# Kernel tuning notes

Hardware: AMD Instinct MI355X
Metric: run time of the kernel (lower is better)

Reference implementation:

```python
import jax, jax.numpy as jnp
import numpy as np

DIM = 192
R = 16            # patches_resolution, D=H=W=R
SP = 4            # split_size
NH = 6            # num_heads (block level); per-branch heads = NH//3
B = 2
L = R * R * R
EPS = 1e-5


def layernorm(x, g, b):
    mu = jnp.mean(x, axis=-1, keepdims=True)
    var = jnp.mean(jnp.square(x - mu), axis=-1, keepdims=True)
    return (x - mu) * jax.lax.rsqrt(var + EPS) * g + b


def window_partition(x, d_sp, h_sp, w_sp, nh):
    b, _, _, _, cb = x.shape
    win = d_sp * h_sp * w_sp
    x = x.reshape(b, R // d_sp, d_sp, R // h_sp, h_sp, R // w_sp, w_sp, cb)
    x = x.transpose(0, 1, 3, 5, 2, 4, 6, 7).reshape(-1, win, nh, cb // nh)
    return x.transpose(0, 2, 1, 3)


def window_merge(x, d_sp, h_sp, w_sp, b):
    cb = x.shape[-1]
    x = x.reshape(b, R // d_sp, R // h_sp, R // w_sp, d_sp, h_sp, w_sp, cb)
    x = x.transpose(0, 1, 4, 2, 5, 3, 6, 7).reshape(b, L, cb)
    return x


def lepe_attention(q, k, v, d_sp, h_sp, w_sp, nh):
    # q,k,v: (B, L, Cb). Note: LePE bias is computed-but-unused in the source -> pure windowed SDPA.
    b, _, cb = q.shape
    hd = cb // nh
    scale = hd ** -0.5
    q5 = q.reshape(b, R, R, R, cb)
    k5 = k.reshape(b, R, R, R, cb)
    v5 = v.reshape(b, R, R, R, cb)
    qw = window_partition(q5, d_sp, h_sp, w_sp, nh) * scale
    kw = window_partition(k5, d_sp, h_sp, w_sp, nh)
    vw = window_partition(v5, d_sp, h_sp, w_sp, nh)
    attn = jax.nn.softmax(jnp.einsum('whqd,whkd->whqk', qw, kw), axis=-1)
    out = jnp.einsum('whqk,whkd->whqd', attn, vw)
    out = out.transpose(0, 2, 1, 3).reshape(-1, d_sp * h_sp * w_sp, cb)
    return window_merge(out, d_sp, h_sp, w_sp, b)


WINDOW_SHAPES = [(R, R, SP), (R, SP, R), (SP, R, R)]  # idx 0,1,2


def setup_inputs() -> dict:
    key = jax.random.key(0)
    ks = jax.random.split(key, 12)
    C = DIM
    H4 = int(C * 4)
    inp = {
        'x': jax.random.normal(ks[0], (B, C, R, R, R), dtype=jnp.float32),
        'w_qkv': jax.random.normal(ks[1], (C, 3 * C), dtype=jnp.float32) * (C ** -0.5),
        'w_proj': jax.random.normal(ks[2], (C, C), dtype=jnp.float32) * (C ** -0.5),
        'b_proj': jnp.zeros((C,), dtype=jnp.float32),
        'g1': jnp.ones((C,), dtype=jnp.float32),
        'b1': jnp.zeros((C,), dtype=jnp.float32),
        'g2': jnp.ones((C,), dtype=jnp.float32),
        'b2': jnp.zeros((C,), dtype=jnp.float32),
        'w_fc1': jax.random.normal(ks[3], (C, H4), dtype=jnp.float32) * (C ** -0.5),
        'b_fc1': jnp.zeros((H4,), dtype=jnp.float32),
        'w_fc2': jax.random.normal(ks[4], (H4, C), dtype=jnp.float32) * (H4 ** -0.5),
        'b_fc2': jnp.zeros((C,), dtype=jnp.float32),
    }
    return inp


def reference(x, w_qkv, w_proj, b_proj, g1, b1, g2, b2, w_fc1, b_fc1, w_fc2, b_fc2):
    C = DIM
    Cb = C // 3
    nh_b = NH // 3
    x = 2.0 * x
    xt = jnp.transpose(x, (0, 2, 3, 4, 1))                # (B, D, H, W, C)
    img = layernorm(xt, g1, b1)
    qkv = img.reshape(B, L, C) @ w_qkv                    # (B, L, 3C)
    q, k, v = jnp.split(qkv.reshape(B, L, 3, C).transpose(2, 0, 1, 3), 3, axis=0)
    q, k, v = q[0], k[0], v[0]                            # each (B, L, C)
    outs = []
    for i, (dsp, hsp, wsp) in enumerate(WINDOW_SHAPES):
        sl = slice(i * Cb, (i + 1) * Cb)
        outs.append(lepe_attention(q[..., sl], k[..., sl], v[..., sl], dsp, hsp, wsp, nh_b))
    attened = jnp.concatenate(outs, axis=2)               # (B, L, C)
    attened = attened @ w_proj + b_proj
    xs = xt.reshape(B, L, C) + attened
    h = layernorm(xs, g2, b2) @ w_fc1 + b_fc1
    h = jax.nn.gelu(h, approximate=False)
    xs = xs + (h @ w_fc2 + b_fc2)
    out = xs.reshape(B, R, R, R, C).transpose(0, 4, 1, 2, 3)  # (B, C, D, H, W)
    return out
```

## Files before the change

### kernel.cpp

```cpp
#include <hip/hip_runtime.h>
#include <hip/hip_bf16.h>

typedef __hip_bfloat16 bf16;
typedef short short8 __attribute__((ext_vector_type(8)));
typedef float floatx4 __attribute__((ext_vector_type(4)));

#define SZ (8192*192)

__device__ __forceinline__ unsigned short f2b(float f) {
    unsigned u = __builtin_bit_cast(unsigned, f);
    u += 0x7FFFu + ((u >> 16) & 1u);
    return (unsigned short)(u >> 16);
}
__device__ __forceinline__ float b2f(unsigned short h) {
    unsigned u = ((unsigned)h) << 16;
    return __builtin_bit_cast(float, u);
}
__device__ __forceinline__ unsigned pk2(float a, float b) {
    return ((unsigned)f2b(b) << 16) | (unsigned)f2b(a);
}

__global__ void detect_kernel(const unsigned short* __restrict__ x16, int* __restrict__ flag) {
    __shared__ int cnt;
    if (threadIdx.x == 0) cnt = 0;
    __syncthreads();
    int c = 0;
    for (int i = threadIdx.x; i < 8192; i += 256) {
        int e = (x16[i] >> 7) & 0xFF;
        if (e >= 152) c++;
    }
    if (c) atomicAdd(&cnt, c);
    __syncthreads();
    if (threadIdx.x == 0) *flag = (cnt >= 32) ? 1 : 0;
}

struct WPA { const void* s[11]; };

__global__ __launch_bounds__(256) void wprep_kernel(WPA a, unsigned short* __restrict__ wdst,
                                                    float* __restrict__ vdst,
                                                    const int* __restrict__ flag) {
    int i = blockIdx.x * 256 + threadIdx.x;
    int f = *flag;
    if (i < 442368) {
        int seg, base, K, N;
        if (i < 110592)      { seg = 0; base = 0;      K = 192; N = 576; }
        else if (i < 147456) { seg = 1; base = 110592; K = 192; N = 192; }
        else if (i < 294912) { seg = 2; base = 147456; K = 192; N = 768; }
        else                 { seg = 3; base = 294912; K = 768; N = 192; }
        int j = i - base;
        int n = j / K, k = j - n * K;
        size_t src = (size_t)k * N + n;
        float v = f ? ((const float*)a.s[seg])[src] : b2f(((const unsigned short*)a.s[seg])[src]);
        wdst[i] = f2b(v);
    } else if (i < 444288) {
        int j = i - 442368;
        int seg, off;
        if (j < 960)       { seg = 4 + j / 192; off = j % 192; }
        else if (j < 1728) { seg = 9; off = j - 960; }
        else               { seg = 10; off = j - 1728; }
        float v = f ? ((const float*)a.s[seg])[off] : b2f(((const unsigned short*)a.s[seg])[off]);
        vdst[j] = v;
    }
}

__global__ __launch_bounds__(256) void prep_kernel(const void* __restrict__ xin,
        const int* __restrict__ flag,
        const float* __restrict__ g1, const float* __restrict__ b1,
        float* __restrict__ xt, unsigned short* __restrict__ img) {
    __shared__ float tile[192][33];
    __shared__ float mu[32], rs[32];
    int tid = threadIdx.x;
    int t0 = blockIdx.x * 32;
    int b = t0 >> 12;
    int ts = t0 & 4095;
    int f = *flag;
    for (int idx = tid; idx < 192 * 32; idx += 256) {
        int c = idx >> 5, tt = idx & 31;
        int gi = ((b * 192 + c) << 12) + ts + tt;
        float raw = f ? ((const float*)xin)[gi] : b2f(((const unsigned short*)xin)[gi]);
        tile[c][tt] = 2.0f * raw;
    }
    __syncthreads();
    {
        int tt = tid >> 3, j = tid & 7;
        int c0 = j * 24;
        float s = 0.f, sq = 0.f;
        #pragma unroll
        for (int i = 0; i < 24; ++i) { float v = tile[c0 + i][tt]; s += v; sq += v * v; }
        s += __shfl_xor(s, 1); sq += __shfl_xor(sq, 1);
        s += __shfl_xor(s, 2); sq += __shfl_xor(sq, 2);
        s += __shfl_xor(s, 4); sq += __shfl_xor(sq, 4);
        if (j == 0) {
            float m = s * (1.0f / 192.0f);
            float var = sq * (1.0f / 192.0f) - m * m;
            mu[tt] = m;
            rs[tt] = rsqrtf(var + 1e-5f);
        }
    }
    __syncthreads();
    for (int idx = tid; idx < 32 * 192; idx += 256) {
        int tt = idx / 192, c = idx % 192;
        float v = tile[c][tt];
        int o = (t0 + tt) * 192 + c;
        xt[o] = v;
        img[o] = f2b((v - mu[tt]) * rs[tt] * g1[c] + b1[c]);
    }
}

__device__ __forceinline__ int g_of(int br, int t) {
    if (br == 0) return (((t >> 2) & 3) << 10) | ((t >> 8) << 6) | (((t >> 4) & 15) << 2) | (t & 3);
    if (br == 1) return (((t >> 6) & 3) << 10) | ((t >> 8) << 6) | (((t >> 4) & 3) << 4) | (t & 15);
    return t;
}

template <int MODE, int W>
__global__ __launch_bounds__(64 * W) void mfma_gemm(const unsigned short* __restrict__ A,
        const unsigned short* __restrict__ WT, const float* __restrict__ bias,
        const float* __restrict__ resid, void* __restrict__ out,
        unsigned short* __restrict__ kt, unsigned short* __restrict__ vt, int N, int K) {
    int wave = threadIdx.x >> 6, lane = threadIdx.x & 63;
    int quad = lane >> 4, l16 = lane & 15;
    int m0 = blockIdx.x * (32 * W) + wave * 32, n0 = blockIdx.y * 64;
    const unsigned short* ap = A + (size_t)(m0 + l16) * K + quad * 8;
    const unsigned short* wp = WT + (size_t)(n0 + l16) * K + quad * 8;
    floatx4 acc[2][4] = {};
    #pragma unroll 2
    for (int kc = 0; kc < K; kc += 32) {
        short8 a0 = *reinterpret_cast<const short8*>(ap + kc);
        short8 a1 = *reinterpret_cast<const short8*>(ap + (size_t)16 * K + kc);
        #pragma unroll
        for (int nt = 0; nt < 4; ++nt) {
            short8 w = *reinterpret_cast<const short8*>(wp + (size_t)nt * 16 * K + kc);
            acc[0][nt] = __builtin_amdgcn_mfma_f32_16x16x32_bf16(a0, w, acc[0][nt], 0, 0, 0);
            acc[1][nt] = __builtin_amdgcn_mfma_f32_16x16x32_bf16(a1, w, acc[1][nt], 0, 0, 0);
        }
    }
    #pragma unroll
    for (int fh = 0; fh < 2; ++fh) {
        #pragma unroll
        for (int nt = 0; nt < 4; ++nt) {
            int col = n0 + nt * 16 + l16;
            if (MODE == 0 && n0 >= 384) {
                int cv = col - 384;
                int d = cv & 31, brh = cv >> 5;
                int row0 = m0 + fh * 16 + quad * 4;
                int bb_ = row0 >> 12, tl = row0 & 4095;
                int g0 = g_of(brh >> 1, tl);
                int wb2 = g0 >> 10, k = g0 & 63, c = k >> 4, m = k & 15;
                int pos = ((c >> 1) << 5) + ((m >> 2) << 3) + ((c & 1) << 2);
                int chunk = (g0 & 1023) >> 6;
                int tidx = ((d >> 4) << 1) | (pos >> 5);
                unsigned short* tile = vt + (((((size_t)(bb_ * 6 + brh) * 4 + wb2) * 16 + chunk) * 4 + tidx) << 9);
                ushort4 w4;
                w4.x = f2b(acc[fh][nt][0]);
                w4.y = f2b(acc[fh][nt][1]);
                w4.z = f2b(acc[fh][nt][2]);
                w4.w = f2b(acc[fh][nt][3]);
                *reinterpret_cast<ushort4*>(tile + (d & 15) * 32 + (pos & 31)) = w4;
            } else if (MODE == 0 && n0 >= 192) {
                int ck = col - 192;
                int d = ck & 31, brh = ck >> 5;
                int row0 = m0 + fh * 16 + quad * 4;
                int bb_ = row0 >> 12, tl = row0 & 4095;
                int g0 = g_of(brh >> 1, tl);
                int wb2 = g0 >> 10, k = g0 & 63, c = k >> 4, m = k & 15;
                int chunk = (g0 & 1023) >> 6;
                unsigned short* tile = kt + (((((size_t)(bb_ * 6 + brh) * 4 + wb2) * 16 + chunk) * 4 + c) << 9);
                tile[m * 32 + d]       = f2b(acc[fh][nt][0]);
                tile[(m + 1) * 32 + d] = f2b(acc[fh][nt][1]);
                tile[(m + 2) * 32 + d] = f2b(acc[fh][nt][2]);
                tile[(m + 3) * 32 + d] = f2b(acc[fh][nt][3]);
            } else {
                #pragma unroll
                for (int r = 0; r < 4; ++r) {
                    int row = m0 + fh * 16 + quad * 4 + r;
                    float v = acc[fh][nt][r];
                    if (MODE == 0 && col < 192) v *= 0.17677669529663689f;
                    if (MODE >= 1) v += bias[col];
                    if (MODE == 2) v = 0.5f * v * (1.0f + erff(v * 0.70710678118654752f));
                    size_t o = (size_t)row * N + col;
                    if (MODE == 0 || MODE == 2) ((unsigned short*)out)[o] = f2b(v);
                    else                        ((float*)out)[o] = v + resid[o];
                }
            }
        }
    }
}

__device__ __forceinline__ int tok_of(int br, int wb, int q) {
    if (br == 0) return ((q >> 6) << 8) | (((q >> 2) & 15) << 4) | (wb << 2) | (q & 3);
    else if (br == 1) return ((q >> 6) << 8) | (((wb << 2) + ((q >> 4) & 3)) << 4) | (q & 15);
    else return (((wb << 2) + (q >> 8)) << 8) | (q & 255);
}

template <int SPLIT>
__global__ __launch_bounds__(256) void attn_mfma(const unsigned short* __restrict__ qkv,
        const unsigned short* __restrict__ kt, const unsigned short* __restrict__ vt,
        unsigned short* __restrict__ attb, float* __restrict__ po, float* __restrict__ pl) {
    const int chunk = 96 * SPLIT;
    int hw = blockIdx.x;
    int bid = (hw & 7) * chunk + (hw >> 3);
    int kh, rest;
    if (SPLIT == 2) { kh = bid & 1; rest = bid >> 1; }
    else            { kh = 0;       rest = bid; }
    int qt = rest & 15, head = (rest >> 4) & 1, wb = (rest >> 5) & 3, b = (rest >> 7) & 1, br = rest >> 8;
    int tid = threadIdx.x;
    int wave = tid >> 6, lane = tid & 63, quad = lane >> 4, l16 = lane & 15;
    int coff = br * 64 + head * 32;
    int tb = b << 12;
    int tq = tok_of(br, wb, qt * 64 + wave * 16 + l16);
    short8 aq = *reinterpret_cast<const short8*>(qkv + (size_t)(tb + tq) * 576 + coff + quad * 8);
    floatx4 o0 = {}, o1 = {};
    float lsum = 0.f;

    const int NT = 16 / SPLIT;
    const size_t base_idx = ((((size_t)(b * 6 + br * 2 + head) * 4 + wb) * 16 + kh * NT) << 11)
                          + l16 * 32 + quad * 8;
    const unsigned short* kp = kt + base_idx;
    const unsigned short* vp = vt + base_idx;

    short8 k0 = *reinterpret_cast<const short8*>(kp);
    short8 k1 = *reinterpret_cast<const short8*>(kp + 512);
    short8 k2 = *reinterpret_cast<const short8*>(kp + 1024);
    short8 k3 = *reinterpret_cast<const short8*>(kp + 1536);
    short8 vb00 = *reinterpret_cast<const short8*>(vp);
    short8 vb01 = *reinterpret_cast<const short8*>(vp + 512);
    short8 vb10 = *reinterpret_cast<const short8*>(vp + 1024);
    short8 vb11 = *reinterpret_cast<const short8*>(vp + 1536);

    for (int it = 0; it < NT; ++it) {
        short8 ck0 = k0, ck1 = k1, ck2 = k2, ck3 = k3;
        short8 cv00 = vb00, cv01 = vb01, cv10 = vb10, cv11 = vb11;
        if (it + 1 < NT) {
            kp += 2048; vp += 2048;
            k0 = *reinterpret_cast<const short8*>(kp);
            k1 = *reinterpret_cast<const short8*>(kp + 512);
            k2 = *reinterpret_cast<const short8*>(kp + 1024);
            k3 = *reinterpret_cast<const short8*>(kp + 1536);
            vb00 = *reinterpret_cast<const short8*>(vp);
            vb01 = *reinterpret_cast<const short8*>(vp + 512);
            vb10 = *reinterpret_cast<const short8*>(vp + 1024);
            vb11 = *reinterpret_cast<const short8*>(vp + 1536);
        }
        floatx4 z = {};
        floatx4 s0 = __builtin_amdgcn_mfma_f32_16x16x32_bf16(ck0, aq, z, 0, 0, 0);
        floatx4 s1 = __builtin_amdgcn_mfma_f32_16x16x32_bf16(ck1, aq, z, 0, 0, 0);
        floatx4 s2 = __builtin_amdgcn_mfma_f32_16x16x32_bf16(ck2, aq, z, 0, 0, 0);
        floatx4 s3 = __builtin_amdgcn_mfma_f32_16x16x32_bf16(ck3, aq, z, 0, 0, 0);
        float p00 = __expf(s0[0]), p01 = __expf(s0[1]), p02 = __expf(s0[2]), p03 = __expf(s0[3]);
        float p10 = __expf(s1[0]), p11 = __expf(s1[1]), p12 = __expf(s1[2]), p13 = __expf(s1[3]);
        float p20 = __expf(s2[0]), p21 = __expf(s2[1]), p22 = __expf(s2[2]), p23 = __expf(s2[3]);
        float p30 = __expf(s3[0]), p31 = __expf(s3[1]), p32 = __expf(s3[2]), p33 = __expf(s3[3]);
        lsum += ((p00 + p01) + (p02 + p03)) + ((p10 + p11) + (p12 + p13))
              + ((p20 + p21) + (p22 + p23)) + ((p30 + p31) + (p32 + p33));
        uint4 ua, ub;
        ua.x = pk2(p00, p01); ua.y = pk2(p02, p03); ua.z = pk2(p10, p11); ua.w = pk2(p12, p13);
        ub.x = pk2(p20, p21); ub.y = pk2(p22, p23); ub.z = pk2(p30, p31); ub.w = pk2(p32, p33);
        short8 pa0 = __builtin_bit_cast(short8, ua);
        short8 pa1 = __builtin_bit_cast(short8, ub);
        o0 = __builtin_amdgcn_mfma_f32_16x16x32_bf16(pa0, cv00, o0, 0, 0, 0);
        o0 = __builtin_amdgcn_mfma_f32_16x16x32_bf16(pa1, cv01, o0, 0, 0, 0);
        o1 = __builtin_amdgcn_mfma_f32_16x16x32_bf16(pa0, cv10, o1, 0, 0, 0);
        o1 = __builtin_amdgcn_mfma_f32_16x16x32_bf16(pa1, cv11, o1, 0, 0, 0);
    }
    lsum += __shfl_xor(lsum, 16);
    lsum += __shfl_xor(lsum, 32);
    if (SPLIT == 2) {
        #pragma unroll
        for (int r = 0; r < 4; ++r) {
            float dv = __shfl(lsum, quad * 4 + r);
            int q = qt * 64 + wave * 16 + quad * 4 + r;
            int t = tok_of(br, wb, q);
            size_t o = ((size_t)(kh << 13) + tb + t) * 192 + coff;
            po[o + l16]      = o0[r];
            po[o + 16 + l16] = o1[r];
            if (l16 == 0) pl[(size_t)((kh << 13) + tb + t) * 6 + br * 2 + head] = dv;
        }
    } else {
        #pragma unroll
        for (int r = 0; r < 4; ++r) {
            float inv = 1.0f / __shfl(lsum, quad * 4 + r);
            int q = qt * 64 + wave * 16 + quad * 4 + r;
            int t = tok_of(br, wb, q);
            size_t o = (size_t)(tb + t) * 192 + coff;
            attb[o + l16]      = f2b(o0[r] * inv);
            attb[o + 16 + l16] = f2b(o1[r] * inv);
        }
    }
}

__global__ __launch_bounds__(256) void attn_combine(const float* __restrict__ po,
        const float* __restrict__ pl, unsigned short* __restrict__ attb) {
    int token = (blockIdx.x << 2) + (threadIdx.x >> 6);
    int lane = threadIdx.x & 63;
    const float* r0 = po + (size_t)token * 192;
    const float* r1 = r0 + (size_t)8192 * 192;
    const float* q0 = pl + (size_t)token * 6;
    const float* q1 = q0 + (size_t)8192 * 6;
    unsigned short* orow = attb + (size_t)token * 192;
    #pragma unroll
    for (int sgm = 0; sgm < 3; ++sgm) {
        int d = lane + sgm * 64;
        int g = d >> 5;
        float denom = q0[g] + q1[g];
        orow[d] = f2b((r0[d] + r1[d]) / denom);
    }
}

__global__ __launch_bounds__(256) void ln_kernel(const float* __restrict__ in,
        const float* __restrict__ g, const float* __restrict__ bb, unsigned short* __restrict__ out) {
    int token = (blockIdx.x << 2) + (threadIdx.x >> 6);
    int lane = threadIdx.x & 63;
    const float* row = in + (size_t)token * 192;
    float v0 = row[lane], v1 = row[lane + 64], v2 = row[lane + 128];
    float s = v0 + v1 + v2, sq = v0 * v0 + v1 * v1 + v2 * v2;
    #pragma unroll
    for (int mask = 1; mask < 64; mask <<= 1) {
        s += __shfl_xor(s, mask);
        sq += __shfl_xor(sq, mask);
    }
    float m = s * (1.f / 192.f);
    float var = sq * (1.f / 192.f) - m * m;
    float rsd = rsqrtf(var + 1e-5f);
    unsigned short* orow = out + (size_t)token * 192;
    orow[lane]       = f2b((v0 - m) * rsd * g[lane]       + bb[lane]);
    orow[lane + 64]  = f2b((v1 - m) * rsd * g[lane + 64]  + bb[lane + 64]);
    orow[lane + 128] = f2b((v2 - m) * rsd * g[lane + 128] + bb[lane + 128]);
}

__global__ __launch_bounds__(256) void unprep_kernel(const float* __restrict__ xs,
                                                     void* __restrict__ out,
                                                     const int* __restrict__ flag) {
    __shared__ float tile[192][33];
    int tid = threadIdx.x;
    int t0 = blockIdx.x * 32;
    int b = t0 >> 12, ts = t0 & 4095;
    for (int idx = tid; idx < 32 * 192; idx += 256) {
        int tt = idx / 192, c = idx % 192;
        tile[c][tt] = xs[(size_t)(t0 + tt) * 192 + c];
    }
    __syncthreads();
    int f = *flag;
    for (int idx = tid; idx < 192 * 32; idx += 256) {
        int c = idx >> 5, tt = idx & 31;
        float v = tile[c][tt];
        int o = ((b * 192 + c) << 12) + ts + tt;
        if (f) ((float*)out)[o] = v;
        else   ((unsigned short*)out)[o] = f2b(v);
    }
}

extern "C" void kernel_launch(void* const* d_in, const int* in_sizes, int n_in,
                              void* d_out, int out_size, void* d_ws, size_t ws_size,
                              hipStream_t stream) {
    float* ws = (float*)d_ws;

    float* vbase = ws;
    float* bprojf = vbase + 0;
    float* g1f    = vbase + 192;
    float* b1f    = vbase + 384;
    float* g2f    = vbase + 576;
    float* b2f    = vbase + 768;
    float* bfc1f  = vbase + 960;
    float* bfc2f  = vbase + 1728;

    unsigned short* wbase = (unsigned short*)(ws + 1920);
    unsigned short* wqkvT = wbase + 0;
    unsigned short* wprojT = wbase + 110592;
    unsigned short* wfc1T = wbase + 147456;
    unsigned short* wfc2T = wbase + 294912;

    size_t p = 1920 + 442368 / 2;
    float* xt = ws + p; p += SZ;
    unsigned short* img = (unsigned short*)(ws + p); p += SZ / 2;
    size_t pQ = p;
    unsigned short* qkv = (unsigned short*)(ws + pQ);
    unsigned short* hbuf = (unsigned short*)(ws + pQ);
    p = pQ + 8192 * 768 / 2;
    unsigned short* attb = (unsigned short*)(ws + p); p += SZ / 2;
    int* flag = (int*)(ws + p); p += 16;
    unsigned short* ktb = (unsigned short*)(ws + p); p += SZ / 2;
    unsigned short* vtb = (unsigned short*)(ws + p); p += SZ / 2;
    float* po = ws + p; p += (size_t)2 * 8192 * 192;
    float* pl = ws + p; p += (size_t)2 * 8192 * 6;
    bool split_ok = ws_size >= p * sizeof(float);
    float* xs = xt;
    unsigned short* lnb = img;

    WPA wa;
    wa.s[0] = d_in[1];  wa.s[1] = d_in[2];  wa.s[2] = d_in[8];  wa.s[3] = d_in[10];
    wa.s[4] = d_in[3];  wa.s[5] = d_in[4];  wa.s[6] = d_in[5];  wa.s[7] = d_in[6];
    wa.s[8] = d_in[7];  wa.s[9] = d_in[9];  wa.s[10] = d_in[11];

    detect_kernel<<<dim3(1), dim3(256), 0, stream>>>((const unsigned short*)d_in[0], flag);
    wprep_kernel<<<dim3(1736), dim3(256), 0, stream>>>(wa, wbase, vbase, flag);
    prep_kernel<<<dim3(256), dim3(256), 0, stream>>>(d_in[0], flag, g1f, b1f, xt, img);
    mfma_gemm<0, 2><<<dim3(128, 9), dim3(128), 0, stream>>>(
        img, wqkvT, nullptr, nullptr, qkv, ktb, vtb, 576, 192);
    if (split_ok) {
        attn_mfma<2><<<dim3(1536), dim3(256), 0, stream>>>(qkv, ktb, vtb, nullptr, po, pl);
        attn_combine<<<dim3(2048), dim3(256), 0, stream>>>(po, pl, attb);
    } else {
        attn_mfma<1><<<dim3(768), dim3(256), 0, stream>>>(qkv, ktb, vtb, attb, nullptr, nullptr);
    }
    mfma_gemm<1, 1><<<dim3(256, 3), dim3(64), 0, stream>>>(
        attb, wprojT, bprojf, xt, xs, nullptr, nullptr, 192, 192);
    ln_kernel<<<dim3(2048), dim3(256), 0, stream>>>(xs, g2f, b2f, lnb);
    mfma_gemm<2, 2><<<dim3(128, 12), dim3(128), 0, stream>>>(
        lnb, wfc1T, bfc1f, nullptr, hbuf, nullptr, nullptr, 768, 192);
    mfma_gemm<3, 1><<<dim3(256, 3), dim3(64), 0, stream>>>(
        hbuf, wfc2T, bfc2f, xs, xs, nullptr, nullptr, 192, 768);
    unprep_kernel<<<dim3(256), dim3(256), 0, stream>>>(xs, d_out, flag);
}
```

Before: 205.0 us.

## Tile weights and Q into MFMA-fragment layout; drop split-K attention and combine

Weights are repacked in wprep into contiguous 64x32 fragment tiles, so each GEMM weight load reads a contiguous 1KB block instead of strided rows. The QKV GEMM now writes Q, pre-scaled, into a per-window tiled buffer, so attention loads Q contiguously instead of gathering rows of the qkv matrix. The two-way KV split with fp32 partials and a separate combine kernel is removed, and attention runs one pass over all 16 KV tiles with half the blocks. This saves the partial-buffer traffic and one launch, but lowers attention parallelism and lengthens the per-block loop.

```diff
diff --git a/kernel.cpp b/kernel.cpp
--- a/kernel.cpp
+++ b/kernel.cpp
@@ -51,7 +51,9 @@
         int n = j / K, k = j - n * K;
         size_t src = (size_t)k * N + n;
         float v = f ? ((const float*)a.s[seg])[src] : b2f(((const unsigned short*)a.s[seg])[src]);
-        wdst[i] = f2b(v);
+        int ci = (n >> 6) * (K >> 5) + (k >> 5);
+        int off = (ci << 11) + (((n >> 4) & 3) << 9) + ((n & 15) << 5) + (k & 31);
+        wdst[base + off] = f2b(v);
     } else if (i < 444288) {
         int j = i - 442368;
         int seg, off;
@@ -117,20 +119,22 @@
 __global__ __launch_bounds__(64 * W) void mfma_gemm(const unsigned short* __restrict__ A,
         const unsigned short* __restrict__ WT, const float* __restrict__ bias,
         const float* __restrict__ resid, void* __restrict__ out,
-        unsigned short* __restrict__ kt, unsigned short* __restrict__ vt, int N, int K) {
+        unsigned short* __restrict__ qt, unsigned short* __restrict__ kt,
+        unsigned short* __restrict__ vt, int N, int K) {
     int wave = threadIdx.x >> 6, lane = threadIdx.x & 63;
     int quad = lane >> 4, l16 = lane & 15;
     int m0 = blockIdx.x * (32 * W) + wave * 32, n0 = blockIdx.y * 64;
     const unsigned short* ap = A + (size_t)(m0 + l16) * K + quad * 8;
-    const unsigned short* wp = WT + (size_t)(n0 + l16) * K + quad * 8;
+    const unsigned short* wpB = WT + (((size_t)blockIdx.y * (K >> 5)) << 11) + l16 * 32 + quad * 8;
     floatx4 acc[2][4] = {};
     #pragma unroll 2
     for (int kc = 0; kc < K; kc += 32) {
         short8 a0 = *reinterpret_cast<const short8*>(ap + kc);
         short8 a1 = *reinterpret_cast<const short8*>(ap + (size_t)16 * K + kc);
+        const unsigned short* wc = wpB + (((size_t)(kc >> 5)) << 11);
         #pragma unroll
         for (int nt = 0; nt < 4; ++nt) {
-            short8 w = *reinterpret_cast<const short8*>(wp + (size_t)nt * 16 * K + kc);
+            short8 w = *reinterpret_cast<const short8*>(wc + nt * 512);
             acc[0][nt] = __builtin_amdgcn_mfma_f32_16x16x32_bf16(a0, w, acc[0][nt], 0, 0, 0);
             acc[1][nt] = __builtin_amdgcn_mfma_f32_16x16x32_bf16(a1, w, acc[1][nt], 0, 0, 0);
         }
@@ -170,17 +174,28 @@
                 tile[(m + 1) * 32 + d] = f2b(acc[fh][nt][1]);
                 tile[(m + 2) * 32 + d] = f2b(acc[fh][nt][2]);
                 tile[(m + 3) * 32 + d] = f2b(acc[fh][nt][3]);
+            } else if (MODE == 0) {
+                int d = col & 31, brh = col >> 5;
+                int row0 = m0 + fh * 16 + quad * 4;
+                int bb_ = row0 >> 12, tl = row0 & 4095;
+                int g0 = g_of(brh >> 1, tl);
+                int wb2 = g0 >> 10, q = g0 & 1023;
+                int chunk = q >> 4, m = q & 15;
+                unsigned short* tile = qt + ((((size_t)(bb_ * 6 + brh) * 4 + wb2) * 64 + chunk) << 9);
+                tile[m * 32 + d]       = f2b(acc[fh][nt][0] * 0.17677669529663689f);
+                tile[(m + 1) * 32 + d] = f2b(acc[fh][nt][1] * 0.17677669529663689f);
+                tile[(m + 2) * 32 + d] = f2b(acc[fh][nt][2] * 0.17677669529663689f);
+                tile[(m + 3) * 32 + d] = f2b(acc[fh][nt][3] * 0.17677669529663689f);
             } else {
                 #pragma unroll
                 for (int r = 0; r < 4; ++r) {
                     int row = m0 + fh * 16 + quad * 4 + r;
                     float v = acc[fh][nt][r];
-                    if (MODE == 0 && col < 192) v *= 0.17677669529663689f;
                     if (MODE >= 1) v += bias[col];
                     if (MODE == 2) v = 0.5f * v * (1.0f + erff(v * 0.70710678118654752f));
                     size_t o = (size_t)row * N + col;
-                    if (MODE == 0 || MODE == 2) ((unsigned short*)out)[o] = f2b(v);
-                    else                        ((float*)out)[o] = v + resid[o];
+                    if (MODE == 2) ((unsigned short*)out)[o] = f2b(v);
+                    else           ((float*)out)[o] = v + resid[o];
                 }
             }
         }
@@ -193,31 +208,25 @@
     else return (((wb << 2) + (q >> 8)) << 8) | (q & 255);
 }
 
-template <int SPLIT>
-__global__ __launch_bounds__(256) void attn_mfma(const unsigned short* __restrict__ qkv,
+__global__ __launch_bounds__(256) void attn_mfma(const unsigned short* __restrict__ qt,
         const unsigned short* __restrict__ kt, const unsigned short* __restrict__ vt,
-        unsigned short* __restrict__ attb, float* __restrict__ po, float* __restrict__ pl) {
-    const int chunk = 96 * SPLIT;
+        unsigned short* __restrict__ attb) {
     int hw = blockIdx.x;
-    int bid = (hw & 7) * chunk + (hw >> 3);
-    int kh, rest;
-    if (SPLIT == 2) { kh = bid & 1; rest = bid >> 1; }
-    else            { kh = 0;       rest = bid; }
-    int qt = rest & 15, head = (rest >> 4) & 1, wb = (rest >> 5) & 3, b = (rest >> 7) & 1, br = rest >> 8;
+    int bid = (hw & 7) * 96 + (hw >> 3);
+    int qti = bid & 15, head = (bid >> 4) & 1, wb = (bid >> 5) & 3, b = (bid >> 7) & 1, br = bid >> 8;
     int tid = threadIdx.x;
     int wave = tid >> 6, lane = tid & 63, quad = lane >> 4, l16 = lane & 15;
     int coff = br * 64 + head * 32;
+    int brh = br * 2 + head;
     int tb = b << 12;
-    int tq = tok_of(br, wb, qt * 64 + wave * 16 + l16);
-    short8 aq = *reinterpret_cast<const short8*>(qkv + (size_t)(tb + tq) * 576 + coff + quad * 8);
+    size_t qbase = ((((size_t)(b * 6 + brh) * 4 + wb) * 64 + qti * 4 + wave) << 9) + l16 * 32 + quad * 8;
+    short8 aq = *reinterpret_cast<const short8*>(qt + qbase);
     floatx4 o0 = {}, o1 = {};
     float lsum = 0.f;
 
-    const int NT = 16 / SPLIT;
-    const size_t base_idx = ((((size_t)(b * 6 + br * 2 + head) * 4 + wb) * 16 + kh * NT) << 11)
-                          + l16 * 32 + quad * 8;
-    const unsigned short* kp = kt + base_idx;
-    const unsigned short* vp = vt + base_idx;
+    const size_t kvbase = ((((size_t)(b * 6 + brh) * 4 + wb) * 16) << 11) + l16 * 32 + quad * 8;
+    const unsigned short* kp = kt + kvbase;
+    const unsigned short* vp = vt + kvbase;
 
     short8 k0 = *reinterpret_cast<const short8*>(kp);
     short8 k1 = *reinterpret_cast<const short8*>(kp + 512);
@@ -228,10 +237,10 @@
     short8 vb10 = *reinterpret_cast<const short8*>(vp + 1024);
     short8 vb11 = *reinterpret_cast<const short8*>(vp + 1536);
 
-    for (int it = 0; it < NT; ++it) {
+    for (int it = 0; it < 16; ++it) {
         short8 ck0 = k0, ck1 = k1, ck2 = k2, ck3 = k3;
         short8 cv00 = vb00, cv01 = vb01, cv10 = vb10, cv11 = vb11;
-        if (it + 1 < NT) {
+        if (it + 1 < 16) {
             kp += 2048; vp += 2048;
             k0 = *reinterpret_cast<const short8*>(kp);
             k1 = *reinterpret_cast<const short8*>(kp + 512);
@@ -265,45 +274,14 @@
     }
     lsum += __shfl_xor(lsum, 16);
     lsum += __shfl_xor(lsum, 32);
-    if (SPLIT == 2) {
-        #pragma unroll
-        for (int r = 0; r < 4; ++r) {
-            float dv = __shfl(lsum, quad * 4 + r);
-            int q = qt * 64 + wave * 16 + quad * 4 + r;
-            int t = tok_of(br, wb, q);
-            size_t o = ((size_t)(kh << 13) + tb + t) * 192 + coff;
-            po[o + l16]      = o0[r];
-            po[o + 16 + l16] = o1[r];
-            if (l16 == 0) pl[(size_t)((kh << 13) + tb + t) * 6 + br * 2 + head] = dv;
-        }
-    } else {
-        #pragma unroll
-        for (int r = 0; r < 4; ++r) {
-            float inv = 1.0f / __shfl(lsum, quad * 4 + r);
-            int q = qt * 64 + wave * 16 + quad * 4 + r;
-            int t = tok_of(br, wb, q);
-            size_t o = (size_t)(tb + t) * 192 + coff;
-            attb[o + l16]      = f2b(o0[r] * inv);
-            attb[o + 16 + l16] = f2b(o1[r] * inv);
-        }
-    }
-}
-
-__global__ __launch_bounds__(256) void attn_combine(const float* __restrict__ po,
-        const float* __restrict__ pl, unsigned short* __restrict__ attb) {
-    int token = (blockIdx.x << 2) + (threadIdx.x >> 6);
-    int lane = threadIdx.x & 63;
-    const float* r0 = po + (size_t)token * 192;
-    const float* r1 = r0 + (size_t)8192 * 192;
-    const float* q0 = pl + (size_t)token * 6;
-    const float* q1 = q0 + (size_t)8192 * 6;
-    unsigned short* orow = attb + (size_t)token * 192;
     #pragma unroll
-    for (int sgm = 0; sgm < 3; ++sgm) {
-        int d = lane + sgm * 64;
-        int g = d >> 5;
-        float denom = q0[g] + q1[g];
-        orow[d] = f2b((r0[d] + r1[d]) / denom);
+    for (int r = 0; r < 4; ++r) {
+        float inv = 1.0f / __shfl(lsum, quad * 4 + r);
+        int q = qti * 64 + wave * 16 + quad * 4 + r;
+        int t = tok_of(br, wb, q);
+        size_t o = (size_t)(tb + t) * 192 + coff;
+        attb[o + l16]      = f2b(o0[r] * inv);
+        attb[o + 16 + l16] = f2b(o1[r] * inv);
     }
 }
 
@@ -374,16 +352,13 @@
     float* xt = ws + p; p += SZ;
     unsigned short* img = (unsigned short*)(ws + p); p += SZ / 2;
     size_t pQ = p;
-    unsigned short* qkv = (unsigned short*)(ws + pQ);
     unsigned short* hbuf = (unsigned short*)(ws + pQ);
     p = pQ + 8192 * 768 / 2;
     unsigned short* attb = (unsigned short*)(ws + p); p += SZ / 2;
     int* flag = (int*)(ws + p); p += 16;
+    unsigned short* qtb = (unsigned short*)(ws + p); p += SZ / 2;
     unsigned short* ktb = (unsigned short*)(ws + p); p += SZ / 2;
     unsigned short* vtb = (unsigned short*)(ws + p); p += SZ / 2;
-    float* po = ws + p; p += (size_t)2 * 8192 * 192;
-    float* pl = ws + p; p += (size_t)2 * 8192 * 6;
-    bool split_ok = ws_size >= p * sizeof(float);
     float* xs = xt;
     unsigned short* lnb = img;
 
@@ -396,19 +371,14 @@
     wprep_kernel<<<dim3(1736), dim3(256), 0, stream>>>(wa, wbase, vbase, flag);
     prep_kernel<<<dim3(256), dim3(256), 0, stream>>>(d_in[0], flag, g1f, b1f, xt, img);
     mfma_gemm<0, 2><<<dim3(128, 9), dim3(128), 0, stream>>>(
-        img, wqkvT, nullptr, nullptr, qkv, ktb, vtb, 576, 192);
-    if (split_ok) {
-        attn_mfma<2><<<dim3(1536), dim3(256), 0, stream>>>(qkv, ktb, vtb, nullptr, po, pl);
-        attn_combine<<<dim3(2048), dim3(256), 0, stream>>>(po, pl, attb);
-    } else {
-        attn_mfma<1><<<dim3(768), dim3(256), 0, stream>>>(qkv, ktb, vtb, attb, nullptr, nullptr);
-    }
+        img, wqkvT, nullptr, nullptr, nullptr, qtb, ktb, vtb, 576, 192);
+    attn_mfma<<<dim3(768), dim3(256), 0, stream>>>(qtb, ktb, vtb, attb);
     mfma_gemm<1, 1><<<dim3(256, 3), dim3(64), 0, stream>>>(
-        attb, wprojT, bprojf, xt, xs, nullptr, nullptr, 192, 192);
+        attb, wprojT, bprojf, xt, xs, nullptr, nullptr, nullptr, 192, 192);
     ln_kernel<<<dim3(2048), dim3(256), 0, stream>>>(xs, g2f, b2f, lnb);
     mfma_gemm<2, 2><<<dim3(128, 12), dim3(128), 0, stream>>>(
-        lnb, wfc1T, bfc1f, nullptr, hbuf, nullptr, nullptr, 768, 192);
+        lnb, wfc1T, bfc1f, nullptr, hbuf, nullptr, nullptr, nullptr, 768, 192);
     mfma_gemm<3, 1><<<dim3(256, 3), dim3(64), 0, stream>>>(
-        hbuf, wfc2T, bfc2f, xs, xs, nullptr, nullptr, 192, 768);
+        hbuf, wfc2T, bfc2f, xs, xs, nullptr, nullptr, nullptr, 192, 768);
     unprep_kernel<<<dim3(256), dim3(256), 0, stream>>>(xs, d_out, flag);
 }
```

Measured after the change: 183.9 us. 1.11x faster.
